# Optimization experiments

Measured on AMD Instinct MI355X. Metric: run time of the kernel, lower is better.

Reference implementation:

```python
import jax, jax.numpy as jnp
import numpy as np

H = 16       # num heads
D = 80       # head dim
HID = H * D  # 1280
S = 4096     # total tokens


def setup_inputs() -> dict:
    key = jax.random.key(0)
    ks = jax.random.split(key, 6)
    x = jax.random.normal(ks[0], (S, HID), dtype=jnp.float32)
    # 4 images of 1024 patch tokens each
    cu_seqlens = jnp.array([0, 1024, 2048, 3072, 4096], dtype=jnp.int32)
    rotary_pos_emb = jax.random.normal(ks[1], (S, D // 2), dtype=jnp.float32)
    sc = 1.0 / np.sqrt(HID)
    qkv_w = jax.random.normal(ks[2], (3 * HID, HID), dtype=jnp.float32) * sc
    qkv_b = jax.random.normal(ks[3], (3 * HID,), dtype=jnp.float32) * 0.02
    proj_w = jax.random.normal(ks[4], (HID, HID), dtype=jnp.float32) * sc
    proj_b = jax.random.normal(ks[5], (HID,), dtype=jnp.float32) * 0.02
    return {"x": x, "cu_seqlens": cu_seqlens, "rotary_pos_emb": rotary_pos_emb,
            "qkv_w": qkv_w, "qkv_b": qkv_b, "proj_w": proj_w, "proj_b": proj_b}


def _rotate_half(t):
    t1, t2 = jnp.split(t, 2, axis=-1)
    return jnp.concatenate([-t2, t1], axis=-1)


def _apply_rope(t, freqs):
    # t: [S, H, D], freqs: [S, D//2] -> cos/sin broadcast as [S, 1, D]
    emb = jnp.concatenate([freqs, freqs], axis=-1)[:, None, :]
    return t * jnp.cos(emb) + _rotate_half(t) * jnp.sin(emb)


def reference(x, cu_seqlens, rotary_pos_emb, qkv_w, qkv_b, proj_w, proj_b):
    seq_len = x.shape[0]
    qkv = (x @ qkv_w.T + qkv_b).reshape(seq_len, 3, H, D)
    q, k, v = qkv[:, 0], qkv[:, 1], qkv[:, 2]  # each [S, H, D]
    q = _apply_rope(q, rotary_pos_emb)
    k = _apply_rope(k, rotary_pos_emb)
    # block-diagonal mask from cu_seqlens: same segment -> 0, else dtype min
    seg = jnp.searchsorted(cu_seqlens[1:], jnp.arange(seq_len), side='right')
    neg = jnp.finfo(q.dtype).min
    attn_mask = jnp.where(seg[:, None] == seg[None, :], 0.0, neg).astype(q.dtype)
    scores = jnp.einsum('shd,thd->hst', q, k) / jnp.sqrt(jnp.asarray(D, q.dtype))
    scores = scores + attn_mask[None]
    attn = jax.nn.softmax(scores.astype(jnp.float32), axis=-1).astype(q.dtype)
    out = jnp.einsum('hst,thd->shd', attn, v).reshape(seq_len, H * D)
    return out @ proj_w.T + proj_b
```

## Files before the change

### kernel.cpp

```cpp
#include <hip/hip_runtime.h>

typedef _Float16 f16;
typedef __attribute__((ext_vector_type(8))) _Float16 f16x8;
typedef __attribute__((ext_vector_type(4))) float f32x4;

#define SEQ   4096
#define NH    16
#define HD    80
#define HIDN  1280
#define DP    96

#define KSZ   3328
#define VSZ   4480
#define HSZ   (2*KSZ + 2*VSZ)

#define KQ   1280
#define NQ   3840
#define NIT  10

__device__ __forceinline__ void gload16(const void* g, void* l) {
  __builtin_amdgcn_global_load_lds(
      (const __attribute__((address_space(1))) unsigned int*)g,
      (__attribute__((address_space(3))) unsigned int*)l, 16, 0, 0);
}

__device__ __forceinline__ unsigned pk2(float a, float b) {
  return __builtin_bit_cast(unsigned, __builtin_amdgcn_cvt_pkrtz(a, b));
}
__device__ __forceinline__ f16x8 bc16(uint4 u) { return __builtin_bit_cast(f16x8, u); }

#define BAR() __builtin_amdgcn_s_barrier()
#define VMCNT(n) do { asm volatile("s_waitcnt vmcnt(" #n ")" ::: "memory"); \
                      __builtin_amdgcn_sched_barrier(0); } while (0)
#define STG(Lb, g, buf, h, kt)                                                  \
  do {                                                                          \
    gload16((g) + (size_t)((h) * 128) * KQ + (kt) * 64,                         \
            (Lb) + (buf) * 16384 + ((h) * 128) * 64 + w * 512);                 \
    gload16((g) + (size_t)((h) * 128 + 64) * KQ + (kt) * 64,                    \
            (Lb) + (buf) * 16384 + ((h) * 128 + 64) * 64 + w * 512);            \
  } while (0)
#define MFQ(IOFF, JOFF, BB)                                                     \
  do {                                                                          \
    __builtin_amdgcn_s_setprio(1);                                              \
    _Pragma("unroll")                                                           \
    for (int i_ = 0; i_ < 4; i_++)                                              \
      _Pragma("unroll")                                                         \
      for (int j_ = 0; j_ < 2; j_++)                                            \
        _Pragma("unroll")                                                       \
        for (int s_ = 0; s_ < 2; s_++)                                          \
          acc[i_ + IOFF][j_ + JOFF] = __builtin_amdgcn_mfma_f32_16x16x32_f16(   \
              a[i_][s_], BB[j_][s_], acc[i_ + IOFF][j_ + JOFF], 0, 0, 0);       \
    __builtin_amdgcn_s_setprio(0);                                              \
  } while (0)

__global__ __launch_bounds__(256) void cvt3_kernel(const float* __restrict__ s0,
                                                   const float* __restrict__ s1,
                                                   const float* __restrict__ s2,
                                                   f16* __restrict__ d0,
                                                   f16* __restrict__ d1,
                                                   f16* __restrict__ d2,
                                                   int n0, int n1, int n2) {
  long i = (long)(blockIdx.x * 256 + threadIdx.x) * 8;
  const float* s; f16* d;
  if (i < n0)                { s = s0 + i;            d = d0 + i; }
  else if (i < n0 + n1)      { s = s1 + (i - n0);     d = d1 + (i - n0); }
  else if (i < n0 + n1 + n2) { s = s2 + (i - n0 - n1); d = d2 + (i - n0 - n1); }
  else return;
  f32x4 v0 = *(const f32x4*)(s);
  f32x4 v1 = *(const f32x4*)(s + 4);
  f16x8 o;
#pragma unroll
  for (int j = 0; j < 4; j++) { o[j] = (f16)v0[j]; o[4 + j] = (f16)v1[j]; }
  *(f16x8*)(d) = o;
}

__global__ __launch_bounds__(512, 2) void qkv_gemm8(const f16* __restrict__ A,
                                                    const f16* __restrict__ B,
                                                    const float* __restrict__ bias,
                                                    f16* __restrict__ C) {
  __shared__ __align__(16) f16 LA[2 * 16384];
  __shared__ __align__(16) f16 LB[2 * 16384];
  const int tid = threadIdx.x, w = tid >> 6, l = tid & 63;
  const int bid = (blockIdx.x & 7) * 30 + (blockIdx.x >> 3);
  const int bx = bid % 15, by = bid / 15;
  const int m0 = by * 256, n0 = bx * 256;
  const int wm = (w >> 2) * 128, wn = (w & 3) * 64;
  const int fr = l & 15, fq = l >> 4;
  const int rx = fr & 7;
  const int cA0 = (fq ^ rx) * 8;
  const int cA1 = ((4 + fq) ^ rx) * 8;

  const int srow = w * 8 + (l >> 3);
  const int scol = ((l & 7) ^ (l >> 3)) * 8;
  const f16* gA = A + (size_t)(m0 + srow) * KQ + scol;
  const f16* gB = B + (size_t)(n0 + srow) * KQ + scol;

  f32x4 acc[8][4] = {};
  f16x8 a[4][2], b0[2][2], b1[2][2];

  STG(LA, gA, 0, 0, 0); STG(LA, gA, 0, 1, 0);
  STG(LB, gB, 0, 0, 0); STG(LB, gB, 0, 1, 0);
  STG(LB, gB, 1, 0, 1); STG(LB, gB, 1, 1, 1);
  VMCNT(4);
  BAR();

  for (int it = 0; it < NIT; ++it) {
    const int t = 2 * it;
    const bool lastit = (it == NIT - 1);

#pragma unroll
    for (int i = 0; i < 4; i++) {
      a[i][0] = *(const f16x8*)(LA + (wm + i * 16 + fr) * 64 + cA0);
      a[i][1] = *(const f16x8*)(LA + (wm + i * 16 + fr) * 64 + cA1);
    }
#pragma unroll
    for (int j = 0; j < 2; j++) {
      b0[j][0] = *(const f16x8*)(LB + (wn + j * 16 + fr) * 64 + cA0);
      b0[j][1] = *(const f16x8*)(LB + (wn + j * 16 + fr) * 64 + cA1);
    }
    STG(LA, gA, 1, 0, t + 1);
    BAR(); MFQ(0, 0, b0); BAR();

#pragma unroll
    for (int j = 0; j < 2; j++) {
      b1[j][0] = *(const f16x8*)(LB + (wn + 32 + j * 16 + fr) * 64 + cA0);
      b1[j][1] = *(const f16x8*)(LB + (wn + 32 + j * 16 + fr) * 64 + cA1);
    }
    STG(LA, gA, 1, 1, t + 1);
    BAR(); MFQ(0, 2, b1); BAR();

#pragma unroll
    for (int i = 0; i < 4; i++) {
      a[i][0] = *(const f16x8*)(LA + (wm + 64 + i * 16 + fr) * 64 + cA0);
      a[i][1] = *(const f16x8*)(LA + (wm + 64 + i * 16 + fr) * 64 + cA1);
    }
    if (!lastit) { STG(LB, gB, 0, 0, t + 2); }
    BAR(); MFQ(4, 0, b0); BAR();

    if (!lastit) { STG(LB, gB, 0, 1, t + 2); VMCNT(4); }
    else         { VMCNT(0); }
    BAR(); MFQ(4, 2, b1); BAR();

#pragma unroll
    for (int i = 0; i < 4; i++) {
      a[i][0] = *(const f16x8*)(LA + 16384 + (wm + i * 16 + fr) * 64 + cA0);
      a[i][1] = *(const f16x8*)(LA + 16384 + (wm + i * 16 + fr) * 64 + cA1);
    }
#pragma unroll
    for (int j = 0; j < 2; j++) {
      b0[j][0] = *(const f16x8*)(LB + 16384 + (wn + j * 16 + fr) * 64 + cA0);
      b0[j][1] = *(const f16x8*)(LB + 16384 + (wn + j * 16 + fr) * 64 + cA1);
    }
    if (!lastit) { STG(LA, gA, 0, 0, t + 2); }
    BAR(); MFQ(0, 0, b0); BAR();

#pragma unroll
    for (int j = 0; j < 2; j++) {
      b1[j][0] = *(const f16x8*)(LB + 16384 + (wn + 32 + j * 16 + fr) * 64 + cA0);
      b1[j][1] = *(const f16x8*)(LB + 16384 + (wn + 32 + j * 16 + fr) * 64 + cA1);
    }
    if (!lastit) { STG(LA, gA, 0, 1, t + 2); }
    BAR(); MFQ(0, 2, b1); BAR();

#pragma unroll
    for (int i = 0; i < 4; i++) {
      a[i][0] = *(const f16x8*)(LA + 16384 + (wm + 64 + i * 16 + fr) * 64 + cA0);
      a[i][1] = *(const f16x8*)(LA + 16384 + (wm + 64 + i * 16 + fr) * 64 + cA1);
    }
    if (!lastit) { STG(LB, gB, 1, 0, t + 3); }
    BAR(); MFQ(4, 0, b0); BAR();

    if (!lastit) { STG(LB, gB, 1, 1, t + 3); VMCNT(4); }
    BAR(); MFQ(4, 2, b1); BAR();
  }

#pragma unroll
  for (int i = 0; i < 8; i++) {
    const int row = m0 + wm + i * 16 + fq * 4;
#pragma unroll
    for (int j = 0; j < 4; j++) {
      const int col = n0 + wn + j * 16 + fr;
      const float bv = bias[col];
#pragma unroll
      for (int q = 0; q < 4; q++)
        C[(size_t)(row + q) * NQ + col] = (f16)(acc[i][j][q] + bv);
    }
  }
}

template<int OUT_F32>
__global__ __launch_bounds__(256) void gemm_bt64(const f16* __restrict__ A,
                                                 const f16* __restrict__ B,
                                                 const float* __restrict__ bias,
                                                 void* __restrict__ C,
                                                 int M, int N, int K) {
  __shared__ __align__(16) f16 AsF[8192];
  __shared__ __align__(16) f16 BsF[8192];
  const int tid = threadIdx.x;
  const int w = tid >> 6, l = tid & 63;
  const int m0 = blockIdx.y * 128, n0 = blockIdx.x * 128;
  const int wm = (w >> 1) * 64, wn = (w & 1) * 64;
  const int fr = l & 15, fg = (l >> 4) * 8;

  size_t aoff[4], boff[4];
#pragma unroll
  for (int i = 0; i < 4; i++) {
    const int d = i * 256 + tid;
    const int sub = d >> 9, dd = d & 511;
    const int r = dd >> 2, c = (dd & 3) + sub * 4;
    aoff[i] = (size_t)(m0 + r) * K + c * 8;
    boff[i] = (size_t)(n0 + r) * K + c * 8;
  }

  f32x4 acc[4][4] = {};

  for (int k0 = 0; k0 < K; k0 += 64) {
    if (k0) __syncthreads();
#pragma unroll
    for (int i = 0; i < 4; i++) gload16(A + aoff[i] + k0, AsF + (i * 256 + tid) * 8);
#pragma unroll
    for (int i = 0; i < 4; i++) gload16(B + boff[i] + k0, BsF + (i * 256 + tid) * 8);
    __syncthreads();
    f16x8 af[4][2], bf[4][2];
#pragma unroll
    for (int i = 0; i < 4; i++)
#pragma unroll
      for (int s = 0; s < 2; s++) {
        af[i][s] = *(const f16x8*)(AsF + s * 4096 + (wm + i * 16 + fr) * 32 + fg);
        bf[i][s] = *(const f16x8*)(BsF + s * 4096 + (wn + i * 16 + fr) * 32 + fg);
      }
#pragma unroll
    for (int i = 0; i < 4; i++)
#pragma unroll
      for (int j = 0; j < 4; j++)
#pragma unroll
        for (int s = 0; s < 2; s++)
          acc[i][j] = __builtin_amdgcn_mfma_f32_16x16x32_f16(af[i][s], bf[j][s], acc[i][j], 0, 0, 0);
  }

  const int q4 = (l >> 4) * 4;
#pragma unroll
  for (int i = 0; i < 4; i++) {
    const int row = m0 + wm + i * 16 + q4;
#pragma unroll
    for (int j = 0; j < 4; j++) {
      const int col = n0 + wn + j * 16 + fr;
      const float bv = bias[col];
#pragma unroll
      for (int q = 0; q < 4; q++) {
        float v = acc[i][j][q] + bv;
        if (OUT_F32) ((float*)C)[(size_t)(row + q) * N + col] = v;
        else         ((f16*)C)[(size_t)(row + q) * N + col] = (f16)v;
      }
    }
  }
}

#define RPB 1280
__global__ __launch_bounds__(256) void prep_kernel(const f16* __restrict__ qkvb,
                                                   const float* __restrict__ rpe,
                                                   f16* __restrict__ qh,
                                                   f16* __restrict__ kh,
                                                   f16* __restrict__ vt) {
  __shared__ f16 tile[HD][65];
  const int b = blockIdx.x;
  if (b < RPB) {
    const float SCLT = 0.1118033988749895f * 1.4426950408889634f;
    const int t = b * 256 + threadIdx.x;
    const int d8 = (t % 5) * 8;
    const int h = (t / 5) % NH;
    const int s = t / (5 * NH);
    const f32x4 f0 = *(const f32x4*)(rpe + s * 40 + d8);
    const f32x4 f1 = *(const f32x4*)(rpe + s * 40 + d8 + 4);
    const f16* base = qkvb + (size_t)s * (3 * HIDN) + h * HD;
    const f16x8 q0 = *(const f16x8*)(base + d8);
    const f16x8 q1 = *(const f16x8*)(base + 40 + d8);
    const f16x8 k0 = *(const f16x8*)(base + HIDN + d8);
    const f16x8 k1 = *(const f16x8*)(base + HIDN + 40 + d8);
    f16x8 oq0, oq1, ok0, ok1;
#pragma unroll
    for (int j = 0; j < 8; j++) {
      const float fv = (j < 4) ? f0[j] : f1[j - 4];
      float sn, cs;
      __sincosf(fv, &sn, &cs);
      const float a = (float)q0[j], bq = (float)q1[j];
      oq0[j] = (f16)((a * cs - bq * sn) * SCLT);
      oq1[j] = (f16)((bq * cs + a * sn) * SCLT);
      const float ka = (float)k0[j], kb = (float)k1[j];
      ok0[j] = (f16)(ka * cs - kb * sn);
      ok1[j] = (f16)(kb * cs + ka * sn);
    }
    const size_t ob = ((size_t)h * SEQ + s) * DP;
    *(f16x8*)(qh + ob + d8)      = oq0;
    *(f16x8*)(qh + ob + 40 + d8) = oq1;
    *(f16x8*)(kh + ob + d8)      = ok0;
    *(f16x8*)(kh + ob + 40 + d8) = ok1;
    if (d8 == 32) {
      const f16x8 z = {};
      *(f16x8*)(qh + ob + 80) = z; *(f16x8*)(qh + ob + 88) = z;
      *(f16x8*)(kh + ob + 80) = z; *(f16x8*)(kh + ob + 88) = z;
    }
  } else {
    const int bb = b - RPB;
    const int h = bb >> 6;
    const int s0 = (bb & 63) * 64;
    for (int idx = threadIdx.x; idx < 64 * HD; idx += 256) {
      const int sr = idx / HD, d = idx % HD;
      tile[d][sr] = qkvb[(size_t)(s0 + sr) * (3 * HIDN) + 2 * HIDN + h * HD + d];
    }
    __syncthreads();
    for (int idx = threadIdx.x; idx < HD * 64; idx += 256) {
      const int d = idx >> 6, sc = idx & 63;
      const int blk = sc >> 5, s = sc & 31, g = s >> 3, j = s & 7;
      const int act = blk * 32 + ((j < 4) ? (4 * g + j) : (16 + 4 * g + (j - 4)));
      vt[((size_t)h * HD + d) * SEQ + s0 + sc] = tile[d][act];
    }
  }
}

__global__ __launch_bounds__(512, 4) void attn_kernel(const f16* __restrict__ qh,
                                                      const f16* __restrict__ kh,
                                                      const f16* __restrict__ vt,
                                                      const int* __restrict__ cu,
                                                      f16* __restrict__ ao) {
  __shared__ __align__(16) f16 smem[2 * HSZ];
  const int tid = threadIdx.x, w = tid >> 6, l = tid & 63;
  const int grp = w >> 2, wq = w & 3;
  const int bid = blockIdx.x;
  const int g = bid & 63, ib = bid >> 6;
  const int h = g >> 2;
  const int qblk = ((g & 3) * 8 + ib) * 128;
  int seg = 0;
  while (cu[seg + 1] <= qblk) seg++;
  const int kvb = cu[seg], kve = cu[seg + 1];
  const int nt = (kve - kvb + 63) >> 6;
  const int fr = l & 15, fg = (l >> 4) * 8;
  const int row0 = qblk + wq * 32;

  const f16* qb = qh + ((size_t)h * SEQ + row0 + fr) * DP + fg;
  f16x8 aq0[3], aq1[3];
#pragma unroll
  for (int kk = 0; kk < 3; kk++) {
    aq0[kk] = *(const f16x8*)(qb + kk * 32);
    aq1[kk] = *(const f16x8*)(qb + 16 * DP + kk * 32);
  }

  const int k0g = tid / 384, k0r = (tid % 384) / 12, k0c = tid % 12;
  const int k1r = (128 + tid) / 12, k1c = (128 + tid) % 12;
  const int v0g = tid / 320, v0r = (tid % 320) / 4, v0c = tid & 3;
  const int v1r = (192 + tid) >> 2, v1c = (192 + tid) & 3;
  const f16* kp0 = kh + ((size_t)h * SEQ + kvb + k0g * 32 + k0r) * DP + k0c * 8;
  const f16* kp1 = kh + ((size_t)h * SEQ + kvb + 32 + k1r) * DP + k1c * 8;
  const f16* vp0 = vt + ((size_t)h * HD + v0r) * SEQ + kvb + v0g * 32 + v0c * 8;
  const f16* vp1 = vt + ((size_t)h * HD + v1r) * SEQ + kvb + 32 + v1c * 8;
  const int dK0 = k0g * KSZ + k0r * 104 + k0c * 8;
  const int dK1 = KSZ + k1r * 104 + k1c * 8;
  const int dV0 = 2 * KSZ + v0g * VSZ + v0r * 56 + v0c * 8;
  const int dV1 = 2 * KSZ + VSZ + v1r * 56 + v1c * 8;

  float m = -1e30f, ls0 = 0.f, ls1 = 0.f;
  f32x4 o0[5] = {}, o1[5] = {};

  uint4 rk0, rk1, rv0, rv1;
  rk0 = *(const uint4*)kp0;
  if (tid < 256) rk1 = *(const uint4*)kp1;
  rv0 = *(const uint4*)vp0;
  if (tid < 128) rv1 = *(const uint4*)vp1;
  *(uint4*)(smem + dK0) = rk0;
  if (tid < 256) *(uint4*)(smem + dK1) = rk1;
  *(uint4*)(smem + dV0) = rv0;
  if (tid < 128) *(uint4*)(smem + dV1) = rv1;
  __syncthreads();

  for (int t = 0; t < nt; t++) {
    const int p = t & 1;
    const int off = (t + 1) * 64;
    const bool more = (t + 1 < nt);

    if (more) {
      rk0 = *(const uint4*)(kp0 + (size_t)off * DP);
      if (tid < 256) rk1 = *(const uint4*)(kp1 + (size_t)off * DP);
      rv0 = *(const uint4*)(vp0 + off);
      if (tid < 128) rv1 = *(const uint4*)(vp1 + off);
    }

    const f16* myK = smem + p * HSZ + grp * KSZ;
    const f16* myV = smem + p * HSZ + 2 * KSZ + grp * VSZ;

    f32x4 s00 = {0.f,0.f,0.f,0.f}, s10 = {0.f,0.f,0.f,0.f};
    f32x4 s01 = {0.f,0.f,0.f,0.f}, s11 = {0.f,0.f,0.f,0.f};
    __builtin_amdgcn_s_setprio(1);
#pragma unroll
    for (int kk = 0; kk < 3; kk++) {
      const f16x8 k0 = *(const f16x8*)(myK + fr * 104 + kk * 32 + fg);
      const f16x8 k1 = *(const f16x8*)(myK + (16 + fr) * 104 + kk * 32 + fg);
      s00 = __builtin_amdgcn_mfma_f32_16x16x32_f16(k0, aq0[kk], s00, 0, 0, 0);
      s10 = __builtin_amdgcn_mfma_f32_16x16x32_f16(k1, aq0[kk], s10, 0, 0, 0);
      s01 = __builtin_amdgcn_mfma_f32_16x16x32_f16(k0, aq1[kk], s01, 0, 0, 0);
      s11 = __builtin_amdgcn_mfma_f32_16x16x32_f16(k1, aq1[kk], s11, 0, 0, 0);
    }
    __builtin_amdgcn_s_setprio(0);

    float pmax = fmaxf(fmaxf(s00[0], s10[0]), fmaxf(s01[0], s11[0]));
#pragma unroll
    for (int j = 1; j < 4; j++) {
      pmax = fmaxf(pmax, fmaxf(s00[j], s10[j]));
      pmax = fmaxf(pmax, fmaxf(s01[j], s11[j]));
    }
    if (__any(pmax > m + 8.f)) {
      float tmax = pmax;
      tmax = fmaxf(tmax, __shfl_xor(tmax, 1));
      tmax = fmaxf(tmax, __shfl_xor(tmax, 2));
      tmax = fmaxf(tmax, __shfl_xor(tmax, 4));
      tmax = fmaxf(tmax, __shfl_xor(tmax, 8));
      tmax = fmaxf(tmax, __shfl_xor(tmax, 16));
      tmax = fmaxf(tmax, __shfl_xor(tmax, 32));
      const float aa = __builtin_amdgcn_exp2f(m - tmax);
      m = tmax;
      ls0 *= aa; ls1 *= aa;
#pragma unroll
      for (int dt = 0; dt < 5; dt++)
#pragma unroll
        for (int j = 0; j < 4; j++) { o0[dt][j] *= aa; o1[dt][j] *= aa; }
    }

#pragma unroll
    for (int r = 0; r < 4; r++) {
      s00[r] = __builtin_amdgcn_exp2f(s00[r] - m);
      s10[r] = __builtin_amdgcn_exp2f(s10[r] - m);
      s01[r] = __builtin_amdgcn_exp2f(s01[r] - m);
      s11[r] = __builtin_amdgcn_exp2f(s11[r] - m);
      ls0 += s00[r] + s10[r];
      ls1 += s01[r] + s11[r];
    }
    uint4 ua, ub;
    ua.x = pk2(s00[0], s00[1]); ua.y = pk2(s00[2], s00[3]);
    ua.z = pk2(s10[0], s10[1]); ua.w = pk2(s10[2], s10[3]);
    ub.x = pk2(s01[0], s01[1]); ub.y = pk2(s01[2], s01[3]);
    ub.z = pk2(s11[0], s11[1]); ub.w = pk2(s11[2], s11[3]);
    const f16x8 paA = bc16(ua), paB = bc16(ub);

    __builtin_amdgcn_s_setprio(1);
#pragma unroll
    for (int dt = 0; dt < 5; dt++) {
      const f16x8 bv = *(const f16x8*)(myV + (dt * 16 + fr) * 56 + fg);
      o0[dt] = __builtin_amdgcn_mfma_f32_16x16x32_f16(paA, bv, o0[dt], 0, 0, 0);
      o1[dt] = __builtin_amdgcn_mfma_f32_16x16x32_f16(paB, bv, o1[dt], 0, 0, 0);
    }
    __builtin_amdgcn_s_setprio(0);

    if (more) {
      f16* dst = smem + (1 - p) * HSZ;
      *(uint4*)(dst + dK0) = rk0;
      if (tid < 256) *(uint4*)(dst + dK1) = rk1;
      *(uint4*)(dst + dV0) = rv0;
      if (tid < 128) *(uint4*)(dst + dV1) = rv1;
    }
    __syncthreads();
  }

  ls0 += __shfl_xor(ls0, 16); ls0 += __shfl_xor(ls0, 32);
  ls1 += __shfl_xor(ls1, 16); ls1 += __shfl_xor(ls1, 32);

  float* mb = (float*)smem;
  if (grp == 1) {
    float* dst = mb + (wq * 64 + l) * 43;
    dst[0] = m; dst[1] = ls0; dst[2] = ls1;
#pragma unroll
    for (int dt = 0; dt < 5; dt++)
#pragma unroll
      for (int j = 0; j < 4; j++) {
        dst[3 + dt * 4 + j]  = o0[dt][j];
        dst[23 + dt * 4 + j] = o1[dt][j];
      }
  }
  __syncthreads();
  if (grp == 0) {
    const float* src = mb + (wq * 64 + l) * 43;
    const float mB = src[0];
    const float M = fmaxf(m, mB);
    const float aA = __builtin_amdgcn_exp2f(m - M);
    const float aB = __builtin_amdgcn_exp2f(mB - M);
    ls0 = ls0 * aA + src[1] * aB;
    ls1 = ls1 * aA + src[2] * aB;
#pragma unroll
    for (int dt = 0; dt < 5; dt++)
#pragma unroll
      for (int j = 0; j < 4; j++) {
        o0[dt][j] = o0[dt][j] * aA + src[3 + dt * 4 + j] * aB;
        o1[dt][j] = o1[dt][j] * aA + src[23 + dt * 4 + j] * aB;
      }

    const float inv0 = 1.0f / ls0, inv1 = 1.0f / ls1;
    float iv0[4], iv1[4];
#pragma unroll
    for (int j = 0; j < 4; j++) {
      const int srcl = (l & 48) | ((l >> 4) * 4 + j);
      iv0[j] = __shfl(inv0, srcl);
      iv1[j] = __shfl(inv1, srcl);
    }
    const int orow = row0 + (l >> 4) * 4;
#pragma unroll
    for (int dt = 0; dt < 5; dt++)
#pragma unroll
      for (int j = 0; j < 4; j++) {
        ao[(size_t)(orow + j) * HIDN + h * HD + dt * 16 + fr]      = (f16)(o0[dt][j] * iv0[j]);
        ao[(size_t)(orow + 16 + j) * HIDN + h * HD + dt * 16 + fr] = (f16)(o1[dt][j] * iv1[j]);
      }
  }
}

extern "C" void kernel_launch(void* const* d_in, const int* in_sizes, int n_in,
                              void* d_out, int out_size, void* d_ws, size_t ws_size,
                              hipStream_t stream) {
  const float* x      = (const float*)d_in[0];
  const int*   cu     = (const int*)d_in[1];
  const float* rpe    = (const float*)d_in[2];
  const float* qkv_w  = (const float*)d_in[3];
  const float* qkv_b  = (const float*)d_in[4];
  const float* proj_w = (const float*)d_in[5];
  const float* proj_b = (const float*)d_in[6];

  char* ws = (char*)d_ws;
  f16* xb    = (f16*)(ws);
  f16* wqkv  = (f16*)(ws + 10485760);
  f16* wproj = (f16*)(ws + 20316160);
  f16* qkvb  = (f16*)(ws + 23592960);
  f16* qh    = (f16*)(ws + 55050240);
  f16* kh    = (f16*)(ws + 67633152);
  f16* vt    = (f16*)(ws + 80216064);
  f16* ao    = xb;

  const int n0 = SEQ * HIDN, n1 = 3 * HIDN * HIDN, n2 = HIDN * HIDN;
  cvt3_kernel<<<(n0 + n1 + n2) / (256 * 8), 256, 0, stream>>>(
      x, qkv_w, proj_w, xb, wqkv, wproj, n0, n1, n2);

  qkv_gemm8<<<240, 512, 0, stream>>>(xb, wqkv, qkv_b, qkvb);

  prep_kernel<<<RPB + 1024, 256, 0, stream>>>(qkvb, rpe, qh, kh, vt);

  attn_kernel<<<512, 512, 0, stream>>>(qh, kh, vt, cu, ao);

  gemm_bt64<1><<<dim3(HIDN / 128, SEQ / 128), 256, 0, stream>>>(
      ao, wproj, proj_b, d_out, SEQ, HIDN, HIDN);
}
```

Before: 137.5 us.

## Double attention query tile per block to 256 rows for more K/V reuse

Each attention block now handles 256 query rows instead of 128, so each wave owns 64 rows (four 16-row MFMA tiles) and every K/V tile loaded into shared memory is reused across twice as many queries. The grid halves to 256 blocks and launch bounds drop to 2 blocks per SM to make room for the larger register footprint. The cross-group merge at the end is split into two passes through shared memory. The trade-off is fewer blocks and lower occupancy on a large-CU GPU, plus higher register pressure and possible spills.

Result: faster. 132.8 us (-3.4%).

```diff
diff --git a/kernel.cpp b/kernel.cpp
--- a/kernel.cpp
+++ b/kernel.cpp
@@ -318,7 +318,7 @@
   }
 }
 
-__global__ __launch_bounds__(512, 4) void attn_kernel(const f16* __restrict__ qh,
+__global__ __launch_bounds__(512, 2) void attn_kernel(const f16* __restrict__ qh,
                                                       const f16* __restrict__ kh,
                                                       const f16* __restrict__ vt,
                                                       const int* __restrict__ cu,
@@ -329,21 +329,21 @@
   const int bid = blockIdx.x;
   const int g = bid & 63, ib = bid >> 6;
   const int h = g >> 2;
-  const int qblk = ((g & 3) * 8 + ib) * 128;
+  const int qblk = ((g & 3) * 4 + ib) * 256;
   int seg = 0;
   while (cu[seg + 1] <= qblk) seg++;
   const int kvb = cu[seg], kve = cu[seg + 1];
   const int nt = (kve - kvb + 63) >> 6;
   const int fr = l & 15, fg = (l >> 4) * 8;
-  const int row0 = qblk + wq * 32;
+  const int row0 = qblk + wq * 64;
 
   const f16* qb = qh + ((size_t)h * SEQ + row0 + fr) * DP + fg;
-  f16x8 aq0[3], aq1[3];
-#pragma unroll
-  for (int kk = 0; kk < 3; kk++) {
-    aq0[kk] = *(const f16x8*)(qb + kk * 32);
-    aq1[kk] = *(const f16x8*)(qb + 16 * DP + kk * 32);
-  }
+  f16x8 aq[4][3];
+#pragma unroll
+  for (int u = 0; u < 4; u++)
+#pragma unroll
+    for (int kk = 0; kk < 3; kk++)
+      aq[u][kk] = *(const f16x8*)(qb + u * 16 * DP + kk * 32);
 
   const int k0g = tid / 384, k0r = (tid % 384) / 12, k0c = tid % 12;
   const int k1r = (128 + tid) / 12, k1c = (128 + tid) % 12;
@@ -358,8 +358,9 @@
   const int dV0 = 2 * KSZ + v0g * VSZ + v0r * 56 + v0c * 8;
   const int dV1 = 2 * KSZ + VSZ + v1r * 56 + v1c * 8;
 
-  float m = -1e30f, ls0 = 0.f, ls1 = 0.f;
-  f32x4 o0[5] = {}, o1[5] = {};
+  float m = -1e30f;
+  float ls[4] = {0.f, 0.f, 0.f, 0.f};
+  f32x4 o[4][5] = {};
 
   uint4 rk0, rk1, rv0, rv1;
   rk0 = *(const uint4*)kp0;
@@ -387,26 +388,26 @@
     const f16* myK = smem + p * HSZ + grp * KSZ;
     const f16* myV = smem + p * HSZ + 2 * KSZ + grp * VSZ;
 
-    f32x4 s00 = {0.f,0.f,0.f,0.f}, s10 = {0.f,0.f,0.f,0.f};
-    f32x4 s01 = {0.f,0.f,0.f,0.f}, s11 = {0.f,0.f,0.f,0.f};
+    f32x4 s[4][2] = {};
     __builtin_amdgcn_s_setprio(1);
 #pragma unroll
     for (int kk = 0; kk < 3; kk++) {
       const f16x8 k0 = *(const f16x8*)(myK + fr * 104 + kk * 32 + fg);
       const f16x8 k1 = *(const f16x8*)(myK + (16 + fr) * 104 + kk * 32 + fg);
-      s00 = __builtin_amdgcn_mfma_f32_16x16x32_f16(k0, aq0[kk], s00, 0, 0, 0);
-      s10 = __builtin_amdgcn_mfma_f32_16x16x32_f16(k1, aq0[kk], s10, 0, 0, 0);
-      s01 = __builtin_amdgcn_mfma_f32_16x16x32_f16(k0, aq1[kk], s01, 0, 0, 0);
-      s11 = __builtin_amdgcn_mfma_f32_16x16x32_f16(k1, aq1[kk], s11, 0, 0, 0);
+#pragma unroll
+      for (int u = 0; u < 4; u++) {
+        s[u][0] = __builtin_amdgcn_mfma_f32_16x16x32_f16(k0, aq[u][kk], s[u][0], 0, 0, 0);
+        s[u][1] = __builtin_amdgcn_mfma_f32_16x16x32_f16(k1, aq[u][kk], s[u][1], 0, 0, 0);
+      }
     }
     __builtin_amdgcn_s_setprio(0);
 
-    float pmax = fmaxf(fmaxf(s00[0], s10[0]), fmaxf(s01[0], s11[0]));
-#pragma unroll
-    for (int j = 1; j < 4; j++) {
-      pmax = fmaxf(pmax, fmaxf(s00[j], s10[j]));
-      pmax = fmaxf(pmax, fmaxf(s01[j], s11[j]));
-    }
+    float pmax = s[0][0][0];
+#pragma unroll
+    for (int u = 0; u < 4; u++)
+#pragma unroll
+      for (int j = 0; j < 4; j++)
+        pmax = fmaxf(pmax, fmaxf(s[u][0][j], s[u][1][j]));
     if (__any(pmax > m + 8.f)) {
       float tmax = pmax;
       tmax = fmaxf(tmax, __shfl_xor(tmax, 1));
@@ -417,35 +418,38 @@
       tmax = fmaxf(tmax, __shfl_xor(tmax, 32));
       const float aa = __builtin_amdgcn_exp2f(m - tmax);
       m = tmax;
-      ls0 *= aa; ls1 *= aa;
-#pragma unroll
-      for (int dt = 0; dt < 5; dt++)
-#pragma unroll
-        for (int j = 0; j < 4; j++) { o0[dt][j] *= aa; o1[dt][j] *= aa; }
-    }
-
-#pragma unroll
-    for (int r = 0; r < 4; r++) {
-      s00[r] = __builtin_amdgcn_exp2f(s00[r] - m);
-      s10[r] = __builtin_amdgcn_exp2f(s10[r] - m);
-      s01[r] = __builtin_amdgcn_exp2f(s01[r] - m);
-      s11[r] = __builtin_amdgcn_exp2f(s11[r] - m);
-      ls0 += s00[r] + s10[r];
-      ls1 += s01[r] + s11[r];
-    }
-    uint4 ua, ub;
-    ua.x = pk2(s00[0], s00[1]); ua.y = pk2(s00[2], s00[3]);
-    ua.z = pk2(s10[0], s10[1]); ua.w = pk2(s10[2], s10[3]);
-    ub.x = pk2(s01[0], s01[1]); ub.y = pk2(s01[2], s01[3]);
-    ub.z = pk2(s11[0], s11[1]); ub.w = pk2(s11[2], s11[3]);
-    const f16x8 paA = bc16(ua), paB = bc16(ub);
+#pragma unroll
+      for (int u = 0; u < 4; u++) {
+        ls[u] *= aa;
+#pragma unroll
+        for (int dt = 0; dt < 5; dt++)
+#pragma unroll
+          for (int j = 0; j < 4; j++) o[u][dt][j] *= aa;
+      }
+    }
+
+    f16x8 pa[4];
+#pragma unroll
+    for (int u = 0; u < 4; u++) {
+#pragma unroll
+      for (int r = 0; r < 4; r++) {
+        s[u][0][r] = __builtin_amdgcn_exp2f(s[u][0][r] - m);
+        s[u][1][r] = __builtin_amdgcn_exp2f(s[u][1][r] - m);
+        ls[u] += s[u][0][r] + s[u][1][r];
+      }
+      uint4 ua;
+      ua.x = pk2(s[u][0][0], s[u][0][1]); ua.y = pk2(s[u][0][2], s[u][0][3]);
+      ua.z = pk2(s[u][1][0], s[u][1][1]); ua.w = pk2(s[u][1][2], s[u][1][3]);
+      pa[u] = bc16(ua);
+    }
 
     __builtin_amdgcn_s_setprio(1);
 #pragma unroll
     for (int dt = 0; dt < 5; dt++) {
       const f16x8 bv = *(const f16x8*)(myV + (dt * 16 + fr) * 56 + fg);
-      o0[dt] = __builtin_amdgcn_mfma_f32_16x16x32_f16(paA, bv, o0[dt], 0, 0, 0);
-      o1[dt] = __builtin_amdgcn_mfma_f32_16x16x32_f16(paB, bv, o1[dt], 0, 0, 0);
+#pragma unroll
+      for (int u = 0; u < 4; u++)
+        o[u][dt] = __builtin_amdgcn_mfma_f32_16x16x32_f16(pa[u], bv, o[u][dt], 0, 0, 0);
     }
     __builtin_amdgcn_s_setprio(0);
 
@@ -459,54 +463,83 @@
     __syncthreads();
   }
 
-  ls0 += __shfl_xor(ls0, 16); ls0 += __shfl_xor(ls0, 32);
-  ls1 += __shfl_xor(ls1, 16); ls1 += __shfl_xor(ls1, 32);
+#pragma unroll
+  for (int u = 0; u < 4; u++) {
+    ls[u] += __shfl_xor(ls[u], 16);
+    ls[u] += __shfl_xor(ls[u], 32);
+  }
 
   float* mb = (float*)smem;
+  float aA = 1.f, aB = 0.f;
   if (grp == 1) {
     float* dst = mb + (wq * 64 + l) * 43;
-    dst[0] = m; dst[1] = ls0; dst[2] = ls1;
-#pragma unroll
-    for (int dt = 0; dt < 5; dt++)
-#pragma unroll
-      for (int j = 0; j < 4; j++) {
-        dst[3 + dt * 4 + j]  = o0[dt][j];
-        dst[23 + dt * 4 + j] = o1[dt][j];
-      }
+    dst[0] = m; dst[1] = ls[0]; dst[2] = ls[1];
+#pragma unroll
+    for (int u = 0; u < 2; u++)
+#pragma unroll
+      for (int dt = 0; dt < 5; dt++)
+#pragma unroll
+        for (int j = 0; j < 4; j++)
+          dst[3 + u * 20 + dt * 4 + j] = o[u][dt][j];
   }
   __syncthreads();
   if (grp == 0) {
     const float* src = mb + (wq * 64 + l) * 43;
     const float mB = src[0];
     const float M = fmaxf(m, mB);
-    const float aA = __builtin_amdgcn_exp2f(m - M);
-    const float aB = __builtin_amdgcn_exp2f(mB - M);
-    ls0 = ls0 * aA + src[1] * aB;
-    ls1 = ls1 * aA + src[2] * aB;
-#pragma unroll
-    for (int dt = 0; dt < 5; dt++)
+    aA = __builtin_amdgcn_exp2f(m - M);
+    aB = __builtin_amdgcn_exp2f(mB - M);
+    ls[0] = ls[0] * aA + src[1] * aB;
+    ls[1] = ls[1] * aA + src[2] * aB;
+#pragma unroll
+    for (int u = 0; u < 2; u++)
+#pragma unroll
+      for (int dt = 0; dt < 5; dt++)
+#pragma unroll
+        for (int j = 0; j < 4; j++)
+          o[u][dt][j] = o[u][dt][j] * aA + src[3 + u * 20 + dt * 4 + j] * aB;
+  }
+  __syncthreads();
+  if (grp == 1) {
+    float* dst = mb + (wq * 64 + l) * 42;
+    dst[0] = ls[2]; dst[1] = ls[3];
+#pragma unroll
+    for (int u = 2; u < 4; u++)
+#pragma unroll
+      for (int dt = 0; dt < 5; dt++)
+#pragma unroll
+        for (int j = 0; j < 4; j++)
+          dst[2 + (u - 2) * 20 + dt * 4 + j] = o[u][dt][j];
+  }
+  __syncthreads();
+  if (grp == 0) {
+    const float* src = mb + (wq * 64 + l) * 42;
+    ls[2] = ls[2] * aA + src[0] * aB;
+    ls[3] = ls[3] * aA + src[1] * aB;
+#pragma unroll
+    for (int u = 2; u < 4; u++)
+#pragma unroll
+      for (int dt = 0; dt < 5; dt++)
+#pragma unroll
+        for (int j = 0; j < 4; j++)
+          o[u][dt][j] = o[u][dt][j] * aA + src[2 + (u - 2) * 20 + dt * 4 + j] * aB;
+
+#pragma unroll
+    for (int u = 0; u < 4; u++) {
+      const float inv = 1.0f / ls[u];
+      float iv[4];
 #pragma unroll
       for (int j = 0; j < 4; j++) {
-        o0[dt][j] = o0[dt][j] * aA + src[3 + dt * 4 + j] * aB;
-        o1[dt][j] = o1[dt][j] * aA + src[23 + dt * 4 + j] * aB;
+        const int srcl = (l & 48) | ((l >> 4) * 4 + j);
+        iv[j] = __shfl(inv, srcl);
       }
-
-    const float inv0 = 1.0f / ls0, inv1 = 1.0f / ls1;
-    float iv0[4], iv1[4];
-#pragma unroll
-    for (int j = 0; j < 4; j++) {
-      const int srcl = (l & 48) | ((l >> 4) * 4 + j);
-      iv0[j] = __shfl(inv0, srcl);
-      iv1[j] = __shfl(inv1, srcl);
-    }
-    const int orow = row0 + (l >> 4) * 4;
-#pragma unroll
-    for (int dt = 0; dt < 5; dt++)
-#pragma unroll
-      for (int j = 0; j < 4; j++) {
-        ao[(size_t)(orow + j) * HIDN + h * HD + dt * 16 + fr]      = (f16)(o0[dt][j] * iv0[j]);
-        ao[(size_t)(orow + 16 + j) * HIDN + h * HD + dt * 16 + fr] = (f16)(o1[dt][j] * iv1[j]);
-      }
+      const int orow = row0 + u * 16 + (l >> 4) * 4;
+#pragma unroll
+      for (int dt = 0; dt < 5; dt++)
+#pragma unroll
+        for (int j = 0; j < 4; j++)
+          ao[(size_t)(orow + j) * HIDN + h * HD + dt * 16 + fr] = (f16)(o[u][dt][j] * iv[j]);
+    }
   }
 }
 
@@ -539,7 +572,7 @@
 
   prep_kernel<<<RPB + 1024, 256, 0, stream>>>(qkvb, rpe, qh, kh, vt);
 
-  attn_kernel<<<512, 512, 0, stream>>>(qh, kh, vt, cu, ao);
+  attn_kernel<<<256, 512, 0, stream>>>(qh, kh, vt, cu, ao);
 
   gemm_bt64<1><<<dim3(HIDN / 128, SEQ / 128), 256, 0, stream>>>(
       ao, wproj, proj_b, d_out, SEQ, HIDN, HIDN);
```
